# Kernel optimization log

Measured on AMD Instinct MI355X. Metric: run time of the kernel, lower is better.

The kernel has to match this reference:

```python
import jax, jax.numpy as jnp
import numpy as np

N, IN_DIM, LAT, K = 32768, 128, 64, 8192
BETA = 1.25


def _linear_params(key, d_in, d_out):
    kw, kb = jax.random.split(key)
    lim = 1.0 / np.sqrt(d_in)
    W = jax.random.uniform(kw, (d_out, d_in), minval=-lim, maxval=lim, dtype=jnp.float32)
    b = jax.random.uniform(kb, (d_out,), minval=-lim, maxval=lim, dtype=jnp.float32)
    return W, b


def setup_inputs() -> dict:
    key = jax.random.key(0)
    ks = jax.random.split(key, 9)
    x = jax.random.normal(ks[0], (N, IN_DIM), dtype=jnp.float32)
    # encoder: 128 -> 256 -> 128 -> 64
    enc_W1, enc_b1 = _linear_params(ks[1], IN_DIM, 256)
    enc_W2, enc_b2 = _linear_params(ks[2], 256, 128)
    enc_W3, enc_b3 = _linear_params(ks[3], 128, LAT)
    # codebook: uniform(-1/K, 1/K)
    emb = jax.random.uniform(ks[4], (K, LAT), minval=-1.0 / K, maxval=1.0 / K, dtype=jnp.float32)
    # decoder: 64 -> 128 -> 256 -> (mu: 128, log_var: 128)
    dec_W1, dec_b1 = _linear_params(ks[5], LAT, 128)
    dec_W2, dec_b2 = _linear_params(ks[6], 128, 256)
    dec_Wmu, dec_bmu = _linear_params(ks[7], 256, IN_DIM)
    dec_Wlv, dec_blv = _linear_params(ks[8], 256, IN_DIM)
    return {
        'x': x,
        'enc_W1': enc_W1, 'enc_b1': enc_b1,
        'enc_W2': enc_W2, 'enc_b2': enc_b2,
        'enc_W3': enc_W3, 'enc_b3': enc_b3,
        'emb': emb,
        'dec_W1': dec_W1, 'dec_b1': dec_b1,
        'dec_W2': dec_W2, 'dec_b2': dec_b2,
        'dec_Wmu': dec_Wmu, 'dec_bmu': dec_bmu,
        'dec_Wlv': dec_Wlv, 'dec_blv': dec_blv,
    }


def reference(x, enc_W1, enc_b1, enc_W2, enc_b2, enc_W3, enc_b3, emb,
              dec_W1, dec_b1, dec_W2, dec_b2, dec_Wmu, dec_bmu, dec_Wlv, dec_blv):
    sg = jax.lax.stop_gradient
    # encoder MLP
    h = jax.nn.relu(x @ enc_W1.T + enc_b1)
    h = jax.nn.relu(h @ enc_W2.T + enc_b2)
    lat = h @ enc_W3.T + enc_b3                      # [N, D]
    # vector quantizer: [N, K] pairwise squared distances
    d = (jnp.sum(lat * lat, axis=1, keepdims=True)
         + jnp.sum(emb * emb, axis=1)
         - 2.0 * lat @ emb.T)
    inds = jnp.argmin(d, axis=1)                     # [N]
    one_hot = jax.nn.one_hot(inds, K, dtype=jnp.float32)   # [N, K]
    q = emb[inds]                                    # gather == one_hot @ emb
    commitment = jnp.mean((sg(q) - lat) ** 2)
    embedding_loss = jnp.mean((q - sg(lat)) ** 2)
    vq_loss = BETA * commitment + embedding_loss
    z = lat + sg(q - lat)                            # straight-through
    # decoder MLP
    h = jax.nn.relu(z @ dec_W1.T + dec_b1)
    h = jax.nn.relu(h @ dec_W2.T + dec_b2)
    x_hat = h @ dec_Wmu.T + dec_bmu
    x_hat_var = h @ dec_Wlv.T + dec_blv
    return x_hat, x_hat_var, one_hot, vq_loss
```

## Files before the change

### kernel.cpp

```cpp
#include <hip/hip_runtime.h>
#include <cfloat>
#include <climits>

#define TPB 256


typedef float f32x4 __attribute__((ext_vector_type(4)));

__device__ __forceinline__ void nt_store4(float* p, float4 v) {
  f32x4 nv;
  nv.x = v.x; nv.y = v.y; nv.z = v.z; nv.w = v.w;
  __builtin_nontemporal_store(nv, reinterpret_cast<f32x4*>(p));
}

__global__ __launch_bounds__(TPB) void wt_kernel(
    const float* __restrict__ W1, const float* __restrict__ W2,
    const float* __restrict__ W3, const float* __restrict__ U1,
    const float* __restrict__ U2, const float* __restrict__ Umu,
    const float* __restrict__ Ulv, float* __restrict__ wt) {
  __shared__ float sB[64 * 68];
  const int b = blockIdx.x;
  const float* src; int R, C, lt; float* dst;
  if (b < 8)       { src = W1;  R = 256; C = 128; dst = wt;          lt = b; }
  else if (b < 16) { src = W2;  R = 128; C = 256; dst = wt + 32768;  lt = b - 8; }
  else if (b < 18) { src = W3;  R = 64;  C = 128; dst = wt + 65536;  lt = b - 16; }
  else if (b < 20) { src = U1;  R = 128; C = 64;  dst = wt + 73728;  lt = b - 18; }
  else if (b < 28) { src = U2;  R = 256; C = 128; dst = wt + 81920;  lt = b - 20; }
  else if (b < 36) { src = Umu; R = 128; C = 256; dst = wt + 114688; lt = b - 28; }
  else             { src = Ulv; R = 128; C = 256; dst = wt + 147456; lt = b - 36; }
  const int tiles_r = R >> 6;
  const int r0 = (lt % tiles_r) << 6, c0 = (lt / tiles_r) << 6;
  const int t = threadIdx.x;
  for (int v = t; v < 1024; v += TPB) {
    const int c4 = v & 15, r = v >> 4;
    const float4 w =
        *reinterpret_cast<const float4*>(src + (size_t)(r0 + r) * C + c0 + 4 * c4);
    *reinterpret_cast<float4*>(&sB[r * 68 + 4 * c4]) = w;
  }
  __syncthreads();
  for (int v = t; v < 1024; v += TPB) {
    const int r4 = v & 15, c = v >> 4;
    float4 o;
    o.x = sB[(4 * r4 + 0) * 68 + c];
    o.y = sB[(4 * r4 + 1) * 68 + c];
    o.z = sB[(4 * r4 + 2) * 68 + c];
    o.w = sB[(4 * r4 + 3) * 68 + c];
    *reinterpret_cast<float4*>(dst + (size_t)(c0 + c) * R + r0 + 4 * r4) = o;
  }
}

__global__ __launch_bounds__(TPB) void embt_kernel(const float* __restrict__ emb,
                                                   float* __restrict__ embT,
                                                   float* __restrict__ En) {
  __shared__ float sB[64 * 68];
  const int c0 = blockIdx.x * 64;
  const int t = threadIdx.x;
  for (int v = t; v < 1024; v += TPB) {
    const int d4 = v & 15, r = v >> 4;
    const float4 e =
        *reinterpret_cast<const float4*>(emb + (size_t)(c0 + r) * 64 + 4 * d4);
    *reinterpret_cast<float4*>(&sB[r * 68 + 4 * d4]) = e;
  }
  __syncthreads();
  if (t < 64) {
    const float* row = &sB[t * 68];
    float q[8];
#pragma unroll
    for (int j = 0; j < 8; ++j) q[j] = __fmul_rn(row[j], row[j]);
#pragma unroll
    for (int m = 1; m < 8; ++m)
#pragma unroll
      for (int j = 0; j < 8; ++j) {
        const float v = row[m * 8 + j];
        q[j] = __fadd_rn(q[j], __fmul_rn(v, v));
      }
    En[c0 + t] = __fadd_rn(
        __fadd_rn(__fadd_rn(q[0], q[1]), __fadd_rn(q[2], q[3])),
        __fadd_rn(__fadd_rn(q[4], q[5]), __fadd_rn(q[6], q[7])));
  }
  for (int v = t; v < 1024; v += TPB) {
    const int r4 = v & 15, d = v >> 4;
    float4 o;
    o.x = sB[(4 * r4 + 0) * 68 + d];
    o.y = sB[(4 * r4 + 1) * 68 + d];
    o.z = sB[(4 * r4 + 2) * 68 + d];
    o.w = sB[(4 * r4 + 3) * 68 + d];
    *reinterpret_cast<float4*>(embT + (size_t)d * 8192 + c0 + 4 * r4) = o;
  }
}

__global__ __launch_bounds__(512) void enc_fused(
    const float* __restrict__ x, const float* __restrict__ WT1,
    const float* __restrict__ WT2, const float* __restrict__ WT3,
    const float* __restrict__ b1, const float* __restrict__ b2,
    const float* __restrict__ b3, float* __restrict__ lat) {
  __shared__ float sX[128 * 68];
  __shared__ float sH1[256 * 68];
  __shared__ float sH2[128 * 68];
  const int t = threadIdx.x;
  const int m0 = blockIdx.x * 64;

  for (int v = t; v < 2048; v += 512) {
    const int k4 = v & 31, r = v >> 5;
    const float4 xv =
        *reinterpret_cast<const float4*>(x + (size_t)(m0 + r) * 128 + 4 * k4);
    float* dst = &sX[(4 * k4) * 68 + r];
    dst[0] = xv.x; dst[68] = xv.y; dst[136] = xv.z; dst[204] = xv.w;
  }
  __syncthreads();

  {
    const int cg8 = (t & 31) * 8, rg4 = (t >> 5) * 4;
    float acc[4][8] = {};
#pragma unroll 8
    for (int k = 0; k < 128; ++k) {
      const float4 a = *reinterpret_cast<const float4*>(&sX[k * 68 + rg4]);
      const float* wr = WT1 + (size_t)k * 256 + cg8;
      const float4 b0 = *reinterpret_cast<const float4*>(wr);
      const float4 b1v = *reinterpret_cast<const float4*>(wr + 4);
      const float av[4] = {a.x, a.y, a.z, a.w};
      const float bv[8] = {b0.x, b0.y, b0.z, b0.w, b1v.x, b1v.y, b1v.z, b1v.w};
#pragma unroll
      for (int i = 0; i < 4; ++i)
#pragma unroll
        for (int j = 0; j < 8; ++j) acc[i][j] = fmaf(av[i], bv[j], acc[i][j]);
    }
#pragma unroll
    for (int j = 0; j < 8; ++j) {
      const int col = cg8 + j;
      const float bj = b1[col];
#pragma unroll
      for (int i = 0; i < 4; ++i) {
        const float h = __fadd_rn(acc[i][j], bj);
        sH1[col * 68 + rg4 + i] = h > 0.f ? h : 0.f;
      }
    }
  }
  __syncthreads();

  {
    const int cg4 = (t & 31) * 4, rg4 = (t >> 5) * 4;
    float acc[4][4] = {};
#pragma unroll 8
    for (int k = 0; k < 256; ++k) {
      const float4 a = *reinterpret_cast<const float4*>(&sH1[k * 68 + rg4]);
      const float4 bb =
          *reinterpret_cast<const float4*>(WT2 + (size_t)k * 128 + cg4);
      const float av[4] = {a.x, a.y, a.z, a.w};
      const float bv[4] = {bb.x, bb.y, bb.z, bb.w};
#pragma unroll
      for (int i = 0; i < 4; ++i)
#pragma unroll
        for (int j = 0; j < 4; ++j) acc[i][j] = fmaf(av[i], bv[j], acc[i][j]);
    }
#pragma unroll
    for (int j = 0; j < 4; ++j) {
      const int col = cg4 + j;
      const float bj = b2[col];
#pragma unroll
      for (int i = 0; i < 4; ++i) {
        const float h = __fadd_rn(acc[i][j], bj);
        sH2[col * 68 + rg4 + i] = h > 0.f ? h : 0.f;
      }
    }
  }
  __syncthreads();

  {
    const int cg4 = (t & 15) * 4, rg2 = (t >> 4) * 2;
    float acc[2][4] = {};
#pragma unroll 8
    for (int k = 0; k < 128; ++k) {
      const float2 a = *reinterpret_cast<const float2*>(&sH2[k * 68 + rg2]);
      const float4 bb =
          *reinterpret_cast<const float4*>(WT3 + (size_t)k * 64 + cg4);
      const float av[2] = {a.x, a.y};
      const float bv[4] = {bb.x, bb.y, bb.z, bb.w};
#pragma unroll
      for (int i = 0; i < 2; ++i)
#pragma unroll
        for (int j = 0; j < 4; ++j) acc[i][j] = fmaf(av[i], bv[j], acc[i][j]);
    }
#pragma unroll
    for (int i = 0; i < 2; ++i) {
      float4 o;
      o.x = __fadd_rn(acc[i][0], b3[cg4 + 0]);
      o.y = __fadd_rn(acc[i][1], b3[cg4 + 1]);
      o.z = __fadd_rn(acc[i][2], b3[cg4 + 2]);
      o.w = __fadd_rn(acc[i][3], b3[cg4 + 3]);
      *reinterpret_cast<float4*>(lat + (size_t)(m0 + rg2 + i) * 64 + cg4) = o;
    }
  }
}

__global__ __launch_bounds__(512, 4) void vqdec_kernel(
    const float* __restrict__ lat, const float* __restrict__ embT,
    const float* __restrict__ En, const float* __restrict__ emb,
    const float* __restrict__ UT1, const float* __restrict__ ub1,
    const float* __restrict__ UT2, const float* __restrict__ ub2,
    const float* __restrict__ UTmu, const float* __restrict__ ubmu,
    const float* __restrict__ UTlv, const float* __restrict__ ublv,
    float* __restrict__ oh, float* __restrict__ xh, float* __restrict__ xv,
    float* __restrict__ lossp) {
  __shared__ float smem[13056];
  __shared__ float snl[64];
  __shared__ int ridx[64];
  __shared__ float lacc;
  const int t = threadIdx.x;
  const int m0 = blockIdx.x * 64;

  {
    float* const sL = smem;
    float* const sE = smem + 4352;
    const int w = t >> 6;
    const int cg = t & 63;
    const int cg4 = cg * 4;
    const int rg8 = w * 8;

    for (int v = t; v < 1024; v += 512) {
      const int r = v >> 4, d4 = v & 15;
      const float4 lv =
          *reinterpret_cast<const float4*>(lat + (size_t)(m0 + r) * 64 + 4 * d4);
      float* dst = &sL[(4 * d4) * 68 + r];
      dst[0] = lv.x; dst[68] = lv.y; dst[136] = lv.z; dst[204] = lv.w;
    }
    if (t == 0) lacc = 0.f;
    float4 st[4];
#pragma unroll
    for (int k = 0; k < 4; ++k) {
      const int v = t + (k << 9);
      const int dq = v >> 6, c4 = v & 63;
      st[k] = *reinterpret_cast<const float4*>(embT + (size_t)dq * 8192 + 4 * c4);
    }
    __syncthreads();
    if (t < 64) {
      float q[8];
#pragma unroll
      for (int j = 0; j < 8; ++j) {
        const float v = sL[j * 68 + t];
        q[j] = __fmul_rn(v, v);
      }
#pragma unroll
      for (int m = 1; m < 8; ++m)
#pragma unroll
        for (int j = 0; j < 8; ++j) {
          const float v = sL[(m * 8 + j) * 68 + t];
          q[j] = __fadd_rn(q[j], __fmul_rn(v, v));
        }
      snl[t] = __fadd_rn(
          __fadd_rn(__fadd_rn(q[0], q[1]), __fadd_rn(q[2], q[3])),
          __fadd_rn(__fadd_rn(q[4], q[5]), __fadd_rn(q[6], q[7])));
    }
    __syncthreads();
    float nl[8];
#pragma unroll
    for (int i = 0; i < 8; ++i) nl[i] = snl[rg8 + i];

    float v1[8];
    int i1[8];
#pragma unroll
    for (int i = 0; i < 8; ++i) { v1[i] = FLT_MAX; i1[i] = INT_MAX; }

    const float4 z = make_float4(0.f, 0.f, 0.f, 0.f);
    float acc[8][4];

    for (int h = 0; h < 64; ++h) {
      const int ch = h >> 1, half = h & 1;
      const int c0 = ch << 8;
#pragma unroll
      for (int k = 0; k < 4; ++k) {
        const int v = t + (k << 9);
        const int dq = v >> 6, c4 = v & 63;
        *reinterpret_cast<float4*>(&sE[dq * 260 + 4 * c4]) = st[k];
      }
      __syncthreads();
      if (half == 0) {
#pragma unroll
        for (int i = 0; i < 8; ++i)
#pragma unroll
          for (int j = 0; j < 4; ++j) acc[i][j] = 0.f;
#pragma unroll
        for (int k = 0; k < 8; ++k) {
          const int v = t + (k << 9);
          const int r = v >> 6, c4 = v & 63;
          nt_store4(oh + (size_t)(m0 + r) * 8192 + c0 + 4 * c4, z);
        }
      }
      if (h < 63) {
        const int hn = h + 1;
        const int cn0 = (hn >> 1) << 8;
        const int dn0 = (hn & 1) << 5;
#pragma unroll
        for (int k = 0; k < 4; ++k) {
          const int v = t + (k << 9);
          const int dq = v >> 6, c4 = v & 63;
          st[k] = *reinterpret_cast<const float4*>(
              embT + (size_t)(dn0 + dq) * 8192 + cn0 + 4 * c4);
        }
      }
      const int d0 = half << 5;
#pragma unroll 4
      for (int d = 0; d < 32; ++d) {
        const int dd = d0 + d;
        const float4 a0 = *reinterpret_cast<const float4*>(&sL[dd * 68 + rg8]);
        const float4 a1 =
            *reinterpret_cast<const float4*>(&sL[dd * 68 + rg8 + 4]);
        const float4 bb = *reinterpret_cast<const float4*>(&sE[d * 260 + cg4]);
        const float av[8] = {a0.x, a0.y, a0.z, a0.w, a1.x, a1.y, a1.z, a1.w};
        const float bv[4] = {bb.x, bb.y, bb.z, bb.w};
#pragma unroll
        for (int i = 0; i < 8; ++i)
#pragma unroll
          for (int j = 0; j < 4; ++j) acc[i][j] = fmaf(av[i], bv[j], acc[i][j]);
      }
      if (half == 1) {
        const float4 EA = *reinterpret_cast<const float4*>(En + c0 + cg4);
        const float Ev[4] = {EA.x, EA.y, EA.z, EA.w};
#pragma unroll
        for (int j = 0; j < 4; ++j) {
          const int c = c0 + cg4 + j;
          const float Ec = Ev[j];
#pragma unroll
          for (int i = 0; i < 8; ++i) {
            const float t1 = __fadd_rn(nl[i], Ec);
            const float s = __fsub_rn(t1, __fmul_rn(2.0f, acc[i][j]));
            if (s < v1[i]) { v1[i] = s; i1[i] = c; }
          }
        }
      }
      __syncthreads();
    }

#pragma unroll
    for (int m = 32; m >= 1; m >>= 1) {
#pragma unroll
      for (int i = 0; i < 8; ++i) {
        const float ov = __shfl_xor(v1[i], m);
        const int oi = __shfl_xor(i1[i], m);
        if (ov < v1[i] || (ov == v1[i] && oi < i1[i])) {
          v1[i] = ov; i1[i] = oi;
        }
      }
    }
    if (cg == 0) {
      float ls = 0.f;
#pragma unroll
      for (int i = 0; i < 8; ++i) {
        ridx[rg8 + i] = i1[i];
        ls += v1[i];
      }
      atomicAdd(&lacc, ls);
    }
    __syncthreads();
    if (t == 0) lossp[blockIdx.x] = lacc;

#pragma unroll
    for (int k = 0; k < 8; ++k) {
      const int v = t + (k << 9);
      const int r = v >> 6, c4 = v & 63;
      const int ind = ridx[r];
      const int g4 = ind >> 2;
      if ((g4 & 63) == c4) {
        float4 o = make_float4(0.f, 0.f, 0.f, 0.f);
        reinterpret_cast<float*>(&o)[ind & 3] = 1.f;
        nt_store4(oh + (size_t)(m0 + r) * 8192 + 4 * g4, o);
      }
    }
  }

  {
    float* const sQ = smem;
    float* const sG1 = smem + 4352;
    float* const sG2 = smem;

    for (int v = t; v < 1024; v += 512) {
      const int k4 = v & 15, r = v >> 4;
      const int id = ridx[r];
      const float4 e =
          *reinterpret_cast<const float4*>(emb + (size_t)id * 64 + 4 * k4);
      float* dst = &sQ[(4 * k4) * 68 + r];
      dst[0] = e.x; dst[68] = e.y; dst[136] = e.z; dst[204] = e.w;
    }
    __syncthreads();

    const int cg4 = (t & 31) * 4, rg4 = (t >> 5) * 4;

    {
      float acc[4][4] = {};
#pragma unroll 8
      for (int k = 0; k < 64; ++k) {
        const float4 a = *reinterpret_cast<const float4*>(&sQ[k * 68 + rg4]);
        const float4 bb =
            *reinterpret_cast<const float4*>(UT1 + (size_t)k * 128 + cg4);
        const float av[4] = {a.x, a.y, a.z, a.w};
        const float bv[4] = {bb.x, bb.y, bb.z, bb.w};
#pragma unroll
        for (int i = 0; i < 4; ++i)
#pragma unroll
          for (int j = 0; j < 4; ++j) acc[i][j] = fmaf(av[i], bv[j], acc[i][j]);
      }
#pragma unroll
      for (int j = 0; j < 4; ++j) {
        const int col = cg4 + j;
        const float bj = ub1[col];
#pragma unroll
        for (int i = 0; i < 4; ++i) {
          const float h = acc[i][j] + bj;
          sG1[col * 68 + rg4 + i] = h > 0.f ? h : 0.f;
        }
      }
    }
    __syncthreads();

    float accA[4][4] = {}, accB[4][4] = {};
#pragma unroll 8
    for (int k = 0; k < 128; ++k) {
      const float4 a = *reinterpret_cast<const float4*>(&sG1[k * 68 + rg4]);
      const float4 bA =
          *reinterpret_cast<const float4*>(UT2 + (size_t)k * 256 + cg4);
      const float4 bB =
          *reinterpret_cast<const float4*>(UT2 + (size_t)k * 256 + 128 + cg4);
      const float av[4] = {a.x, a.y, a.z, a.w};
      const float bAv[4] = {bA.x, bA.y, bA.z, bA.w};
      const float bBv[4] = {bB.x, bB.y, bB.z, bB.w};
#pragma unroll
      for (int i = 0; i < 4; ++i)
#pragma unroll
        for (int j = 0; j < 4; ++j) {
          accA[i][j] = fmaf(av[i], bAv[j], accA[i][j]);
          accB[i][j] = fmaf(av[i], bBv[j], accB[i][j]);
        }
    }
    __syncthreads();

#pragma unroll
    for (int j = 0; j < 4; ++j) {
      const int col = cg4 + j;
      const float bj = ub2[col];
#pragma unroll
      for (int i = 0; i < 4; ++i) {
        const float h = accA[i][j] + bj;
        sG2[col * 68 + rg4 + i] = h > 0.f ? h : 0.f;
      }
    }
    __syncthreads();

    float accH[2][4][4] = {};
#pragma unroll 8
    for (int c = 0; c < 128; ++c) {
      const float4 a = *reinterpret_cast<const float4*>(&sG2[c * 68 + rg4]);
      const float4 bm =
          *reinterpret_cast<const float4*>(UTmu + (size_t)c * 128 + cg4);
      const float4 bl =
          *reinterpret_cast<const float4*>(UTlv + (size_t)c * 128 + cg4);
      const float av[4] = {a.x, a.y, a.z, a.w};
      const float bmv[4] = {bm.x, bm.y, bm.z, bm.w};
      const float blv_[4] = {bl.x, bl.y, bl.z, bl.w};
#pragma unroll
      for (int i = 0; i < 4; ++i)
#pragma unroll
        for (int j = 0; j < 4; ++j) {
          accH[0][i][j] = fmaf(av[i], bmv[j], accH[0][i][j]);
          accH[1][i][j] = fmaf(av[i], blv_[j], accH[1][i][j]);
        }
    }
    __syncthreads();

#pragma unroll
    for (int j = 0; j < 4; ++j) {
      const int col = 128 + cg4 + j;
      const float bj = ub2[col];
#pragma unroll
      for (int i = 0; i < 4; ++i) {
        const float h = accB[i][j] + bj;
        sG2[(cg4 + j) * 68 + rg4 + i] = h > 0.f ? h : 0.f;
      }
    }
    __syncthreads();

#pragma unroll 8
    for (int c = 0; c < 128; ++c) {
      const float4 a = *reinterpret_cast<const float4*>(&sG2[c * 68 + rg4]);
      const float4 bm = *reinterpret_cast<const float4*>(
          UTmu + (size_t)(128 + c) * 128 + cg4);
      const float4 bl = *reinterpret_cast<const float4*>(
          UTlv + (size_t)(128 + c) * 128 + cg4);
      const float av[4] = {a.x, a.y, a.z, a.w};
      const float bmv[4] = {bm.x, bm.y, bm.z, bm.w};
      const float blv_[4] = {bl.x, bl.y, bl.z, bl.w};
#pragma unroll
      for (int i = 0; i < 4; ++i)
#pragma unroll
        for (int j = 0; j < 4; ++j) {
          accH[0][i][j] = fmaf(av[i], bmv[j], accH[0][i][j]);
          accH[1][i][j] = fmaf(av[i], blv_[j], accH[1][i][j]);
        }
    }

#pragma unroll
    for (int i = 0; i < 4; ++i) {
      float4 ov;
      ov.x = accH[0][i][0] + ubmu[cg4 + 0];
      ov.y = accH[0][i][1] + ubmu[cg4 + 1];
      ov.z = accH[0][i][2] + ubmu[cg4 + 2];
      ov.w = accH[0][i][3] + ubmu[cg4 + 3];
      nt_store4(xh + (size_t)(m0 + rg4 + i) * 128 + cg4, ov);
      float4 ov2;
      ov2.x = accH[1][i][0] + ublv[cg4 + 0];
      ov2.y = accH[1][i][1] + ublv[cg4 + 1];
      ov2.z = accH[1][i][2] + ublv[cg4 + 2];
      ov2.w = accH[1][i][3] + ublv[cg4 + 3];
      nt_store4(xv + (size_t)(m0 + rg4 + i) * 128 + cg4, ov2);
    }
  }
}

__global__ void fin_kernel(const float* __restrict__ lossp,
                           float* __restrict__ outp) {
  const int t = threadIdx.x;
  double s = 0.0;
  for (int i = t; i < 512; i += 64) s += (double)lossp[i];
#pragma unroll
  for (int m = 32; m >= 1; m >>= 1) s += __shfl_xor(s, m);
  if (t == 0) *outp = (float)(2.25 * s / (32768.0 * 64.0));
}

extern "C" void kernel_launch(void* const* d_in, const int* in_sizes, int n_in,
                              void* d_out, int out_size, void* d_ws,
                              size_t ws_size, hipStream_t stream) {
  const float* x = (const float*)d_in[0];
  const float* eW1 = (const float*)d_in[1];
  const float* eb1 = (const float*)d_in[2];
  const float* eW2 = (const float*)d_in[3];
  const float* eb2 = (const float*)d_in[4];
  const float* eW3 = (const float*)d_in[5];
  const float* eb3 = (const float*)d_in[6];
  const float* emb = (const float*)d_in[7];
  const float* dW1 = (const float*)d_in[8];
  const float* db1 = (const float*)d_in[9];
  const float* dW2 = (const float*)d_in[10];
  const float* db2 = (const float*)d_in[11];
  const float* dWmu = (const float*)d_in[12];
  const float* dbmu = (const float*)d_in[13];
  const float* dWlv = (const float*)d_in[14];
  const float* dblv = (const float*)d_in[15];

  float* out = (float*)d_out;
  float* xhat = out;
  float* xvar = out + 4194304;
  float* oh = out + 8388608;
  float* lossout = out + 276824064;

  float* lat = (float*)d_ws;
  float* En = lat + 2097152;
  float* lossp = En + 8192;
  int* inds = (int*)(lossp + 512);
  float* embT = (float*)(inds + 32768);
  float* wt = embT + 524288;
  float* wt1 = wt;
  float* wt2 = wt + 32768;
  float* wt3 = wt + 65536;
  float* uwt1 = wt + 73728;
  float* uwt2 = wt + 81920;
  float* uwtmu = wt + 114688;
  float* uwtlv = wt + 147456;

  wt_kernel<<<44, TPB, 0, stream>>>(eW1, eW2, eW3, dW1, dW2, dWmu, dWlv, wt);
  embt_kernel<<<128, TPB, 0, stream>>>(emb, embT, En);
  enc_fused<<<512, 512, 0, stream>>>(x, wt1, wt2, wt3, eb1, eb2, eb3, lat);
  vqdec_kernel<<<512, 512, 0, stream>>>(lat, embT, En, emb, uwt1, db1, uwt2,
                                        db2, uwtmu, dbmu, uwtlv, dblv, oh,
                                        xhat, xvar, lossp);
  fin_kernel<<<1, 64, 0, stream>>>(lossp, lossout);
}
```

Measured before the change: 808.5 us.

## Double VQ distance tile to 128 rows and 16x8 register micro-tile per thread

Each vqdec block now handles 128 rows instead of 64, with each thread computing a 16x8 accumulator tile over 512-column codebook chunks instead of 8x4 over 256. The goal is to halve how often the codebook is re-read per row and to raise the FMA-to-LDS-load ratio in the distance GEMM. The decoder runs twice per block over 64-row halves, and the grid halves to 256 blocks with launch bounds lowered to 2. The costs are much higher register pressure (128 accumulators), fewer blocks than 256 CUs may leave parallelism thin, and possible spills.

After: 933.1 us. 15.4% more time.

```diff
diff --git a/kernel.cpp b/kernel.cpp
--- a/kernel.cpp
+++ b/kernel.cpp
@@ -193,7 +193,7 @@
   }
 }
 
-__global__ __launch_bounds__(512, 4) void vqdec_kernel(
+__global__ __launch_bounds__(512, 2) void vqdec_kernel(
     const float* __restrict__ lat, const float* __restrict__ embT,
     const float* __restrict__ En, const float* __restrict__ emb,
     const float* __restrict__ UT1, const float* __restrict__ ub1,
@@ -202,49 +202,49 @@
     const float* __restrict__ UTlv, const float* __restrict__ ublv,
     float* __restrict__ oh, float* __restrict__ xh, float* __restrict__ xv,
     float* __restrict__ lossp) {
-  __shared__ float smem[13056];
-  __shared__ float snl[64];
-  __shared__ int ridx[64];
+  __shared__ float smem[24960];
+  __shared__ float snl[128];
+  __shared__ int ridx[128];
   __shared__ float lacc;
   const int t = threadIdx.x;
-  const int m0 = blockIdx.x * 64;
+  const int m0 = blockIdx.x * 128;
 
   {
     float* const sL = smem;
-    float* const sE = smem + 4352;
+    float* const sE = smem + 8448;
     const int w = t >> 6;
-    const int cg = t & 63;
-    const int cg4 = cg * 4;
-    const int rg8 = w * 8;
-
-    for (int v = t; v < 1024; v += 512) {
+    const int lane = t & 63;
+    const int rg16 = w * 16;
+    const int ln8 = lane * 8;
+
+    for (int v = t; v < 2048; v += 512) {
       const int r = v >> 4, d4 = v & 15;
       const float4 lv =
           *reinterpret_cast<const float4*>(lat + (size_t)(m0 + r) * 64 + 4 * d4);
-      float* dst = &sL[(4 * d4) * 68 + r];
-      dst[0] = lv.x; dst[68] = lv.y; dst[136] = lv.z; dst[204] = lv.w;
+      float* dst = &sL[(4 * d4) * 132 + r];
+      dst[0] = lv.x; dst[132] = lv.y; dst[264] = lv.z; dst[396] = lv.w;
     }
     if (t == 0) lacc = 0.f;
-    float4 st[4];
-#pragma unroll
-    for (int k = 0; k < 4; ++k) {
+    float4 st[8];
+#pragma unroll
+    for (int k = 0; k < 8; ++k) {
       const int v = t + (k << 9);
-      const int dq = v >> 6, c4 = v & 63;
+      const int dq = v >> 7, c4 = v & 127;
       st[k] = *reinterpret_cast<const float4*>(embT + (size_t)dq * 8192 + 4 * c4);
     }
     __syncthreads();
-    if (t < 64) {
+    if (t < 128) {
       float q[8];
 #pragma unroll
       for (int j = 0; j < 8; ++j) {
-        const float v = sL[j * 68 + t];
+        const float v = sL[j * 132 + t];
         q[j] = __fmul_rn(v, v);
       }
 #pragma unroll
       for (int m = 1; m < 8; ++m)
 #pragma unroll
         for (int j = 0; j < 8; ++j) {
-          const float v = sL[(m * 8 + j) * 68 + t];
+          const float v = sL[(m * 8 + j) * 132 + t];
           q[j] = __fadd_rn(q[j], __fmul_rn(v, v));
         }
       snl[t] = __fadd_rn(
@@ -252,76 +252,81 @@
           __fadd_rn(__fadd_rn(q[4], q[5]), __fadd_rn(q[6], q[7])));
     }
     __syncthreads();
-    float nl[8];
-#pragma unroll
-    for (int i = 0; i < 8; ++i) nl[i] = snl[rg8 + i];
-
-    float v1[8];
-    int i1[8];
-#pragma unroll
-    for (int i = 0; i < 8; ++i) { v1[i] = FLT_MAX; i1[i] = INT_MAX; }
+    float nl[16];
+#pragma unroll
+    for (int i = 0; i < 16; ++i) nl[i] = snl[rg16 + i];
+
+    float v1[16];
+    int i1[16];
+#pragma unroll
+    for (int i = 0; i < 16; ++i) { v1[i] = FLT_MAX; i1[i] = INT_MAX; }
 
     const float4 z = make_float4(0.f, 0.f, 0.f, 0.f);
-    float acc[8][4];
-
-    for (int h = 0; h < 64; ++h) {
+    float acc[16][8];
+
+    for (int h = 0; h < 32; ++h) {
       const int ch = h >> 1, half = h & 1;
-      const int c0 = ch << 8;
-#pragma unroll
-      for (int k = 0; k < 4; ++k) {
+      const int c0 = ch << 9;
+#pragma unroll
+      for (int k = 0; k < 8; ++k) {
         const int v = t + (k << 9);
-        const int dq = v >> 6, c4 = v & 63;
-        *reinterpret_cast<float4*>(&sE[dq * 260 + 4 * c4]) = st[k];
+        const int dq = v >> 7, c4 = v & 127;
+        *reinterpret_cast<float4*>(&sE[dq * 516 + 4 * c4]) = st[k];
       }
       __syncthreads();
       if (half == 0) {
 #pragma unroll
-        for (int i = 0; i < 8; ++i)
-#pragma unroll
-          for (int j = 0; j < 4; ++j) acc[i][j] = 0.f;
+        for (int i = 0; i < 16; ++i)
+#pragma unroll
+          for (int j = 0; j < 8; ++j) acc[i][j] = 0.f;
+        const int rz = t >> 7, cz = t & 127;
+#pragma unroll
+        for (int k = 0; k < 32; ++k) {
+          nt_store4(oh + (size_t)(m0 + rz + 4 * k) * 8192 + c0 + 4 * cz, z);
+        }
+      }
+      if (h < 31) {
+        const int hn = h + 1;
+        const int cn0 = (hn >> 1) << 9;
+        const int dn0 = (hn & 1) << 5;
 #pragma unroll
         for (int k = 0; k < 8; ++k) {
           const int v = t + (k << 9);
-          const int r = v >> 6, c4 = v & 63;
-          nt_store4(oh + (size_t)(m0 + r) * 8192 + c0 + 4 * c4, z);
-        }
-      }
-      if (h < 63) {
-        const int hn = h + 1;
-        const int cn0 = (hn >> 1) << 8;
-        const int dn0 = (hn & 1) << 5;
-#pragma unroll
-        for (int k = 0; k < 4; ++k) {
-          const int v = t + (k << 9);
-          const int dq = v >> 6, c4 = v & 63;
+          const int dq = v >> 7, c4 = v & 127;
           st[k] = *reinterpret_cast<const float4*>(
               embT + (size_t)(dn0 + dq) * 8192 + cn0 + 4 * c4);
         }
       }
       const int d0 = half << 5;
-#pragma unroll 4
+#pragma unroll 2
       for (int d = 0; d < 32; ++d) {
         const int dd = d0 + d;
-        const float4 a0 = *reinterpret_cast<const float4*>(&sL[dd * 68 + rg8]);
-        const float4 a1 =
-            *reinterpret_cast<const float4*>(&sL[dd * 68 + rg8 + 4]);
-        const float4 bb = *reinterpret_cast<const float4*>(&sE[d * 260 + cg4]);
-        const float av[8] = {a0.x, a0.y, a0.z, a0.w, a1.x, a1.y, a1.z, a1.w};
-        const float bv[4] = {bb.x, bb.y, bb.z, bb.w};
-#pragma unroll
-        for (int i = 0; i < 8; ++i)
-#pragma unroll
-          for (int j = 0; j < 4; ++j) acc[i][j] = fmaf(av[i], bv[j], acc[i][j]);
+        const float* ap = &sL[dd * 132 + rg16];
+        const float4 a0 = *reinterpret_cast<const float4*>(ap);
+        const float4 a1 = *reinterpret_cast<const float4*>(ap + 4);
+        const float4 a2 = *reinterpret_cast<const float4*>(ap + 8);
+        const float4 a3 = *reinterpret_cast<const float4*>(ap + 12);
+        const float4 b0 = *reinterpret_cast<const float4*>(&sE[d * 516 + ln8]);
+        const float4 b1 =
+            *reinterpret_cast<const float4*>(&sE[d * 516 + ln8 + 4]);
+        const float av[16] = {a0.x, a0.y, a0.z, a0.w, a1.x, a1.y, a1.z, a1.w,
+                              a2.x, a2.y, a2.z, a2.w, a3.x, a3.y, a3.z, a3.w};
+        const float bv[8] = {b0.x, b0.y, b0.z, b0.w, b1.x, b1.y, b1.z, b1.w};
+#pragma unroll
+        for (int i = 0; i < 16; ++i)
+#pragma unroll
+          for (int j = 0; j < 8; ++j) acc[i][j] = fmaf(av[i], bv[j], acc[i][j]);
       }
       if (half == 1) {
-        const float4 EA = *reinterpret_cast<const float4*>(En + c0 + cg4);
-        const float Ev[4] = {EA.x, EA.y, EA.z, EA.w};
-#pragma unroll
-        for (int j = 0; j < 4; ++j) {
-          const int c = c0 + cg4 + j;
+        const float4 EA = *reinterpret_cast<const float4*>(En + c0 + ln8);
+        const float4 EB = *reinterpret_cast<const float4*>(En + c0 + ln8 + 4);
+        const float Ev[8] = {EA.x, EA.y, EA.z, EA.w, EB.x, EB.y, EB.z, EB.w};
+#pragma unroll
+        for (int j = 0; j < 8; ++j) {
+          const int c = c0 + ln8 + j;
           const float Ec = Ev[j];
 #pragma unroll
-          for (int i = 0; i < 8; ++i) {
+          for (int i = 0; i < 16; ++i) {
             const float t1 = __fadd_rn(nl[i], Ec);
             const float s = __fsub_rn(t1, __fmul_rn(2.0f, acc[i][j]));
             if (s < v1[i]) { v1[i] = s; i1[i] = c; }
@@ -334,7 +339,7 @@
 #pragma unroll
     for (int m = 32; m >= 1; m >>= 1) {
 #pragma unroll
-      for (int i = 0; i < 8; ++i) {
+      for (int i = 0; i < 16; ++i) {
         const float ov = __shfl_xor(v1[i], m);
         const int oi = __shfl_xor(i1[i], m);
         if (ov < v1[i] || (ov == v1[i] && oi < i1[i])) {
@@ -342,11 +347,11 @@
         }
       }
     }
-    if (cg == 0) {
+    if (lane == 0) {
       float ls = 0.f;
 #pragma unroll
-      for (int i = 0; i < 8; ++i) {
-        ridx[rg8 + i] = i1[i];
+      for (int i = 0; i < 16; ++i) {
+        ridx[rg16 + i] = i1[i];
         ls += v1[i];
       }
       atomicAdd(&lacc, ls);
@@ -354,28 +359,32 @@
     __syncthreads();
     if (t == 0) lossp[blockIdx.x] = lacc;
 
-#pragma unroll
-    for (int k = 0; k < 8; ++k) {
-      const int v = t + (k << 9);
-      const int r = v >> 6, c4 = v & 63;
-      const int ind = ridx[r];
-      const int g4 = ind >> 2;
-      if ((g4 & 63) == c4) {
-        float4 o = make_float4(0.f, 0.f, 0.f, 0.f);
-        reinterpret_cast<float*>(&o)[ind & 3] = 1.f;
-        nt_store4(oh + (size_t)(m0 + r) * 8192 + 4 * g4, o);
-      }
-    }
-  }
-
-  {
+    {
+      const int rz = t >> 7, cz = t & 127;
+#pragma unroll
+      for (int k = 0; k < 32; ++k) {
+        const int r = rz + 4 * k;
+        const int ind = ridx[r];
+        const int g4 = ind >> 2;
+        if ((g4 & 127) == cz) {
+          float4 o = make_float4(0.f, 0.f, 0.f, 0.f);
+          reinterpret_cast<float*>(&o)[ind & 3] = 1.f;
+          nt_store4(oh + (size_t)(m0 + r) * 8192 + 4 * g4, o);
+        }
+      }
+    }
+  }
+  __syncthreads();
+
+  for (int rh = 0; rh < 2; ++rh) {
+    const int mm0 = m0 + rh * 64;
     float* const sQ = smem;
     float* const sG1 = smem + 4352;
     float* const sG2 = smem;
 
     for (int v = t; v < 1024; v += 512) {
       const int k4 = v & 15, r = v >> 4;
-      const int id = ridx[r];
+      const int id = ridx[rh * 64 + r];
       const float4 e =
           *reinterpret_cast<const float4*>(emb + (size_t)id * 64 + 4 * k4);
       float* dst = &sQ[(4 * k4) * 68 + r];
@@ -504,14 +513,15 @@
       ov.y = accH[0][i][1] + ubmu[cg4 + 1];
       ov.z = accH[0][i][2] + ubmu[cg4 + 2];
       ov.w = accH[0][i][3] + ubmu[cg4 + 3];
-      nt_store4(xh + (size_t)(m0 + rg4 + i) * 128 + cg4, ov);
+      nt_store4(xh + (size_t)(mm0 + rg4 + i) * 128 + cg4, ov);
       float4 ov2;
       ov2.x = accH[1][i][0] + ublv[cg4 + 0];
       ov2.y = accH[1][i][1] + ublv[cg4 + 1];
       ov2.z = accH[1][i][2] + ublv[cg4 + 2];
       ov2.w = accH[1][i][3] + ublv[cg4 + 3];
-      nt_store4(xv + (size_t)(m0 + rg4 + i) * 128 + cg4, ov2);
-    }
+      nt_store4(xv + (size_t)(mm0 + rg4 + i) * 128 + cg4, ov2);
+    }
+    __syncthreads();
   }
 }
 
@@ -519,7 +529,7 @@
                            float* __restrict__ outp) {
   const int t = threadIdx.x;
   double s = 0.0;
-  for (int i = t; i < 512; i += 64) s += (double)lossp[i];
+  for (int i = t; i < 256; i += 64) s += (double)lossp[i];
 #pragma unroll
   for (int m = 32; m >= 1; m >>= 1) s += __shfl_xor(s, m);
   if (t == 0) *outp = (float)(2.25 * s / (32768.0 * 64.0));
@@ -568,7 +578,7 @@
   wt_kernel<<<44, TPB, 0, stream>>>(eW1, eW2, eW3, dW1, dW2, dWmu, dWlv, wt);
   embt_kernel<<<128, TPB, 0, stream>>>(emb, embT, En);
   enc_fused<<<512, 512, 0, stream>>>(x, wt1, wt2, wt3, eb1, eb2, eb3, lat);
-  vqdec_kernel<<<512, 512, 0, stream>>>(lat, embT, En, emb, uwt1, db1, uwt2,
+  vqdec_kernel<<<256, 512, 0, stream>>>(lat, embT, En, emb, uwt1, db1, uwt2,
                                         db2, uwtmu, dbmu, uwtlv, dblv, oh,
                                         xhat, xvar, lossp);
   fin_kernel<<<1, 64, 0, stream>>>(lossp, lossout);
```
